# Optimization experiments

Measured on AMD Instinct MI355X. Metric: run time of the kernel, lower is better.

## Reference

```python
import jax, jax.numpy as jnp
import numpy as np

NITER = 3

def fft2c(x):
    x = jnp.fft.ifftshift(x, axes=(-2, -1))
    x = jnp.fft.fft2(x, axes=(-2, -1), norm='ortho')
    return jnp.fft.fftshift(x, axes=(-2, -1))

def ifft2c(x):
    x = jnp.fft.ifftshift(x, axes=(-2, -1))
    x = jnp.fft.ifft2(x, axes=(-2, -1), norm='ortho')
    return jnp.fft.fftshift(x, axes=(-2, -1))

def conv3d(x, w):
    # x: [N, D, H, W, C]; w: [3,3,3,Cin,Cout]; 'same' padding, stride 1, no bias
    return jax.lax.conv_general_dilated(x, w, window_strides=(1, 1, 1), padding='SAME',
                                        dimension_numbers=('NDHWC', 'DHWIO', 'NDHWC'))

def setup_inputs():
    key = jax.random.key(0)
    ks = jax.random.split(key, 16)
    nb, nt, nx, ny = 1, 18, 160, 160
    s = 0.05  # weight scale to keep unrolled iterations numerically tame
    d_real = jax.random.normal(ks[0], (nb, nt, nx, ny), jnp.float32)
    d_imag = jax.random.normal(ks[1], (nb, nt, nx, ny), jnp.float32)
    mask = jax.random.randint(ks[2], (nt, nx, ny), 0, 2, jnp.int32)
    W1 = jax.random.normal(ks[3], (NITER, 3, 3, 3, 2, 16), jnp.float32) * s
    W2 = jax.random.normal(ks[4], (NITER, 3, 3, 3, 16, 16), jnp.float32) * s
    W3 = jax.random.normal(ks[5], (NITER, 3, 3, 3, 16, 16), jnp.float32) * s
    W4 = jax.random.normal(ks[6], (NITER, 3, 3, 3, 16, 16), jnp.float32) * s
    W5 = jax.random.normal(ks[7], (NITER, 3, 3, 3, 16, 16), jnp.float32) * s
    W6 = jax.random.normal(ks[8], (NITER, 3, 3, 3, 16, 2), jnp.float32) * s
    lam1 = jnp.full((NITER,), 0.1, jnp.float32)       # lambda_step init
    lam2 = jnp.full((NITER,), 0.1, jnp.float32)       # lambda_step_2 init
    soft_thr = jnp.full((NITER,), 0.1, jnp.float32)
    thres_coef = jnp.full((NITER,), -2.0, jnp.float32)
    eta = jnp.full((NITER,), 0.01, jnp.float32)
    return dict(d_real=d_real, d_imag=d_imag, mask=mask, W1=W1, W2=W2, W3=W3, W4=W4,
                W5=W5, W6=W6, lam1=lam1, lam2=lam2, soft_thr=soft_thr,
                thres_coef=thres_coef, eta=eta)

def _slr_net(d_real, d_imag, mask, W1, W2, W3, W4, W5, W6, lam1, lam2, soft_thr, thres_coef, eta):
    d = jax.lax.complex(d_real, d_imag)          # [nb,nt,nx,ny] complex64
    m = mask.astype(jnp.complex64)               # [nt,nx,ny], broadcasts over batch
    x_rec = ifft2c(d * m)                        # E^H d
    t = jnp.zeros_like(x_rec)
    beta = jnp.zeros_like(x_rec)
    X_SYM = []
    for i in range(NITER):
        lam = jnp.maximum(lam1[i], 0.0).astype(jnp.complex64)
        lam2c = jnp.maximum(lam2[i], 0.0).astype(jnp.complex64)
        # data-consistency gradient: E^H (E x - d)
        ATAX = ifft2c(m * (m * fft2c(x_rec) - d))
        r_n = x_rec - lam * ATAX + lam2c * (x_rec + beta - t)
        r = jnp.stack([r_n.real, r_n.imag], axis=-1)  # [nb,nt,nx,ny,2]
        x1 = jax.nn.relu(conv3d(r, W1[i]))
        x2 = jax.nn.relu(conv3d(x1, W2[i]))
        x3 = conv3d(x2, W3[i])
        x_soft = jnp.sign(x3) * jax.nn.relu(jnp.abs(x3) - soft_thr[i])
        x4 = jax.nn.relu(conv3d(x_soft, W4[i]))
        x5 = jax.nn.relu(conv3d(x4, W5[i]))
        x6 = conv3d(x5, W6[i])
        x_out = x6 + r
        xs = jax.nn.relu(conv3d(x3, W4[i]))
        xs = jax.nn.relu(conv3d(xs, W5[i]))
        xs = conv3d(xs, W6[i])
        x_sym = xs - r
        x_rec = jax.lax.complex(x_out[..., 0], x_out[..., 1])
        # low-rank step: batched thin SVD with learned singular-value thresholding
        nb_, nt_, nx_, ny_ = x_rec.shape
        M = x_rec.reshape(nb_, nt_, nx_ * ny_)
        U, S, Vh = jnp.linalg.svd(M, full_matrices=False)   # U:[b,nt,nt] S:[b,nt] Vh:[b,nt,nx*ny]
        thres = jax.nn.sigmoid(thres_coef[i]) * S[:, :1]
        S = jax.nn.relu(S - thres)
        t = (U * S[:, None, :].astype(U.dtype)) @ Vh
        t = t.reshape(nb_, nt_, nx_, ny_)
        beta = beta + jnp.maximum(eta[i], 0.0).astype(jnp.complex64) * (x_rec - t)
        X_SYM.append(x_sym)
    return x_rec, jnp.stack(X_SYM)

def reference(d_real, d_imag, mask, W1, W2, W3, W4, W5, W6, lam1, lam2, soft_thr, thres_coef, eta):
    return _slr_net(d_real, d_imag, mask, W1, W2, W3, W4, W5, W6, lam1, lam2, soft_thr, thres_coef, eta)
```

## Files before the change

kernel.cpp:

```cpp
#include <hip/hip_runtime.h>
#include <hip/hip_fp16.h>

#define NT 18
#define NX 160
#define NY 160
#define NPIX (NX*NY)
#define NVOX (NT*NPIX)

typedef _Float16 __attribute__((ext_vector_type(2))) half2t;
typedef _Float16 __attribute__((ext_vector_type(8))) half8t;
typedef float    __attribute__((ext_vector_type(4))) f32x4;
typedef unsigned int u32;
typedef __attribute__((address_space(1))) const u32 gu32;
typedef __attribute__((address_space(3))) u32 lu32;

__global__ void probe_kernel(float* __restrict__ out, int n, float val) {
  int i = blockIdx.x * 256 + threadIdx.x;
  if (i < n) out[i] = val;
}

__global__ void make_g_kernel(float2* __restrict__ G) {
  int idx = blockIdx.x * 256 + threadIdx.x;
  if (idx >= NPIX) return;
  int r = idx / NY, c = idx - (idx / NY) * NY;
  int rs = (r + 80) % 160;
  int cs = (c + 80) % 160;
  int prod = (rs * cs) % 160;
  double ang = -2.0 * 3.14159265358979323846 * (double)prod / 160.0;
  double sc = 0.07905694150420949;
  G[idx] = make_float2((float)(cos(ang) * sc), (float)(sin(ang) * sc));
}

__global__ void zero_kernel(float* __restrict__ p, int n) {
  int i = blockIdx.x * 256 + threadIdx.x;
  if (i < n) p[i] = 0.f;
}

template <int MASKD>
__global__ void fft_pass_last4(const float2* __restrict__ in, float2* __restrict__ out,
                               const float2* __restrict__ G, int conjf,
                               const float* __restrict__ dr, const float* __restrict__ di,
                               const int* __restrict__ maskp) {
  __shared__ float2 rows[4][NY];
  int r0 = blockIdx.x * 4;
  int v = threadIdx.x;
#pragma unroll
  for (int r = 0; r < 4; ++r) {
    size_t idx = (size_t)(r0 + r) * NY + v;
    if (MASKD) {
      float m = (float)maskp[idx];
      rows[r][v] = make_float2(m * dr[idx], m * di[idx]);
    } else {
      rows[r][v] = in[idx];
    }
  }
  __syncthreads();
  float sgn = conjf ? -1.f : 1.f;
  float ar[4] = {0.f, 0.f, 0.f, 0.f}, ai[4] = {0.f, 0.f, 0.f, 0.f};
  for (int k = 0; k < NY; ++k) {
    float2 g = G[k * NY + v];
    float gi = sgn * g.y;
#pragma unroll
    for (int r = 0; r < 4; ++r) {
      float2 a = rows[r][k];
      ar[r] += a.x * g.x - a.y * gi;
      ai[r] += a.x * gi + a.y * g.x;
    }
  }
#pragma unroll
  for (int r = 0; r < 4; ++r)
    out[(size_t)(r0 + r) * NY + v] = make_float2(ar[r], ai[r]);
}

template <int EPI>
__global__ void fft_pass_mid4(const float2* __restrict__ in, void* __restrict__ outv,
                              const float2* __restrict__ G, int conjf,
                              const float* __restrict__ dr, const float* __restrict__ di,
                              const int* __restrict__ maskp,
                              const float2* __restrict__ xrec2, const float2* __restrict__ beta2,
                              const float2* __restrict__ tbuf2,
                              const float* __restrict__ l1p, const float* __restrict__ l2p) {
  __shared__ float2 grow[4][NX];
  int b = (int)blockIdx.x;
  int sb = (b & 7) * 90 + (b >> 3);
  int t = sb / 40;
  int u0 = (sb - t * 40) * 4;
  int v = threadIdx.x;
#pragma unroll
  for (int r = 0; r < 4; ++r) grow[r][v] = G[(u0 + r) * NX + v];
  __syncthreads();
  float sgn = conjf ? -1.f : 1.f;
  float ar[4] = {0.f, 0.f, 0.f, 0.f}, ai[4] = {0.f, 0.f, 0.f, 0.f};
  const float2* base = in + (size_t)t * NPIX;
  for (int j = 0; j < NX; ++j) {
    float2 a = base[j * NY + v];
#pragma unroll
    for (int r = 0; r < 4; ++r) {
      float2 g = grow[r][j];
      float gi = sgn * g.y;
      ar[r] += a.x * g.x - a.y * gi;
      ai[r] += a.x * gi + a.y * g.x;
    }
  }
  float l1 = 0.f, l2 = 0.f;
  if (EPI == 2) { l1 = fmaxf(l1p[0], 0.f); l2 = fmaxf(l2p[0], 0.f); }
#pragma unroll
  for (int r = 0; r < 4; ++r) {
    size_t idx = (size_t)t * NPIX + (size_t)(u0 + r) * NY + v;
    if (EPI == 0) {
      ((float2*)outv)[idx] = make_float2(ar[r], ai[r]);
    } else if (EPI == 1) {
      float m = (float)maskp[idx];
      ((float2*)outv)[idx] = make_float2(m * (m * ar[r] - dr[idx]),
                                         m * (m * ai[r] - di[idx]));
    } else {
      float2 x = xrec2[idx], bb = beta2[idx], tt = tbuf2[idx];
      ((float*)outv)[2 * idx]     = (1.f + l2) * x.x - l1 * ar[r] + l2 * (bb.x - tt.x);
      ((float*)outv)[2 * idx + 1] = (1.f + l2) * x.y - l1 * ai[r] + l2 * (bb.y - tt.y);
    }
  }
}

template <int MODE>
__device__ void eigen_part(const float2* __restrict__ Ain, float* __restrict__ scr,
                           const float* __restrict__ tcp, float2* __restrict__ Wout) {
  __shared__ float Ar[NT][NT], Ai_[NT][NT], Vr[NT][NT], Vi_[NT][NT];
  __shared__ float cS[9], sS[9], erS[9], eiS[9];
  __shared__ int pS[9], qS[9];
  __shared__ float ratio[NT];
  int tid = threadIdx.x;
  for (int idx = tid; idx < NT * NT; idx += 256) {
    int i = idx / NT, j = idx - (idx / NT) * NT;
    if (MODE == 1) {
      float2 a = Ain[idx];
      Ar[i][j] = a.x;
      Ai_[i][j] = (i == j) ? 0.f : a.y;
      Vr[i][j] = (i == j) ? 1.f : 0.f;
      Vi_[i][j] = 0.f;
    } else {
      Ar[i][j] = scr[idx];
      Ai_[i][j] = scr[324 + idx];
      Vr[i][j] = scr[648 + idx];
      Vi_[i][j] = scr[972 + idx];
    }
  }
  __syncthreads();
  for (int sweep = 0; sweep < 2; ++sweep) {
    for (int r = 0; r < NT - 1; ++r) {
      if (tid < 9) {
        int k = tid;
        int a = (r + k) % (NT - 1);
        int b = (k == 0) ? (NT - 1) : (r - k + (NT - 1)) % (NT - 1);
        int p = min(a, b), q = max(a, b);
        pS[k] = p; qS[k] = q;
        float apr = Ar[p][q], api = Ai_[p][q];
        float r2 = apr * apr + api * api;
        float c = 1.f, s = 0.f, er = 1.f, ei = 0.f;
        if (r2 > 1e-28f) {
          float rr = sqrtf(r2);
          float inv_r = 1.f / rr;
          er = apr * inv_r; ei = api * inv_r;
          float th = (Ar[q][q] - Ar[p][p]) * 0.5f * inv_r;
          float tt = (th >= 0.f ? 1.f : -1.f) / (fabsf(th) + sqrtf(th * th + 1.f));
          c = 1.f / sqrtf(tt * tt + 1.f);
          s = tt * c;
        }
        cS[k] = c; sS[k] = s; erS[k] = er; eiS[k] = ei;
      }
      __syncthreads();
      if (tid < 9 * NT) {
        int idx = tid;
        int k = idx / 9, j = idx - (idx / 9) * 9;
        int p = pS[j], q = qS[j];
        float c = cS[j], s = sS[j], er = erS[j], ei = eiS[j];
        float apr = Ar[k][p], api = Ai_[k][p];
        float aqr = Ar[k][q], aqi = Ai_[k][q];
        float eqr = er * aqr + ei * aqi;
        float eqi = er * aqi - ei * aqr;
        Ar[k][p] = c * apr - s * eqr;  Ai_[k][p] = c * api - s * eqi;
        Ar[k][q] = s * apr + c * eqr;  Ai_[k][q] = s * api + c * eqi;
        float vpr = Vr[k][p], vpi = Vi_[k][p];
        float vqr = Vr[k][q], vqi = Vi_[k][q];
        float evr = er * vqr + ei * vqi;
        float evi = er * vqi - ei * vqr;
        Vr[k][p] = c * vpr - s * evr;  Vi_[k][p] = c * vpi - s * evi;
        Vr[k][q] = s * vpr + c * evr;  Vi_[k][q] = s * vpi + c * evi;
      }
      __syncthreads();
      if (tid < 9 * NT) {
        int idx = tid;
        int k = idx / 9, j = idx - (idx / 9) * 9;
        int p = pS[j], q = qS[j];
        float c = cS[j], s = sS[j], er = erS[j], ei = eiS[j];
        float bpr = Ar[p][k], bpi = Ai_[p][k];
        float bqr = Ar[q][k], bqi = Ai_[q][k];
        float ebr = er * bqr - ei * bqi;
        float ebi = er * bqi + ei * bqr;
        Ar[p][k] = c * bpr - s * ebr;  Ai_[p][k] = c * bpi - s * ebi;
        Ar[q][k] = s * bpr + c * ebr;  Ai_[q][k] = s * bpi + c * ebi;
      }
      __syncthreads();
    }
  }
  if (MODE == 3) {
    if (tid == 0) {
      float smax = 0.f;
      for (int k = 0; k < NT; ++k) {
        float sv = sqrtf(fmaxf(Ar[k][k], 0.f));
        ratio[k] = sv;
        smax = fmaxf(smax, sv);
      }
      float sig = 1.f / (1.f + expf(-tcp[0]));
      float thres = sig * smax;
      for (int k = 0; k < NT; ++k) {
        float sv = ratio[k];
        ratio[k] = (sv > thres) ? (sv - thres) / sv : 0.f;
      }
    }
    __syncthreads();
    for (int idx = tid; idx < NT * NT; idx += 256) {
      int i = idx / NT, j = idx - (idx / NT) * NT;
      float wr = 0.f, wi = 0.f;
      for (int k = 0; k < NT; ++k) {
        float rk = ratio[k];
        wr += rk * (Vr[i][k] * Vr[j][k] + Vi_[i][k] * Vi_[j][k]);
        wi += rk * (Vi_[i][k] * Vr[j][k] - Vr[i][k] * Vi_[j][k]);
      }
      Wout[idx] = make_float2(wr, wi);
    }
  } else {
    for (int idx = tid; idx < NT * NT; idx += 256) {
      int i = idx / NT, j = idx - (idx / NT) * NT;
      scr[idx]       = Ar[i][j];
      scr[324 + idx] = Ai_[i][j];
      scr[648 + idx] = Vr[i][j];
      scr[972 + idx] = Vi_[i][j];
    }
  }
}

#define ROWCH 164
#define NROWS 18
#define NCHUNK (NROWS*ROWCH)

template <int COUT, bool RELU, int OUTMODE, bool SOFT, int EIG>
__global__ void __launch_bounds__(256)
conv3d_mfma_kernel(const __half* __restrict__ in_, const float* __restrict__ wts,
                   void* __restrict__ out_, const float* __restrict__ res, float resSign,
                   const float* __restrict__ thrp,
                   const float2* __restrict__ eigA, float* __restrict__ eigScr,
                   const float* __restrict__ tcp, float2* __restrict__ eigW,
                   float* __restrict__ outReal) {
  if constexpr (EIG > 0) {
    if (blockIdx.x == 0) { eigen_part<EIG>(eigA, eigScr, tcp, eigW); return; }
  }
  __shared__ alignas(16) __half lds[NCHUNK * 8];
  const int tid = threadIdx.x;
  const int bid0 = (EIG > 0) ? ((int)blockIdx.x - 1) : (int)blockIdx.x;
  const int bid = (bid0 & 7) * 180 + (bid0 >> 3);
  const int z   = bid / 80;
  const int rem = bid - z * 80;
  const int y0  = (rem >> 1) * 4;
  const int xbase = (rem & 1) * 80;

  const int lane = tid & 63;
  const int wv = tid >> 6;
  const int n = lane & 15;
  const int g = lane >> 4;
  const int sel = g >> 1;
  const int ci = (g & 1) * 8;

  half8t bw[14];
#pragma unroll
  for (int c = 0; c < 14; ++c) {
#pragma unroll
    for (int j = 0; j < 8; ++j) {
      int kg = c * 32 + g * 8 + j;
      float w = (kg < 432 && n < COUT) ? wts[kg * COUT + n] : 0.f;
      bw[c][j] = (_Float16)w;
    }
  }

  if constexpr (!SOFT) {
    half8t zero8 = {0, 0, 0, 0, 0, 0, 0, 0};
    if (tid < 2 * NROWS) {
      int row = tid >> 1, which = tid & 1;
      int off = (xbase == 0) ? which : (162 + which);
      *reinterpret_cast<half8t*>(&lds[(row * ROWCH + off) * 8]) = zero8;
    }
#pragma unroll 1
    for (int row = 0; row < NROWS; ++row) {
      int zz = z - 1 + row / 6;
      int yy = y0 - 1 + row % 6;
      if ((unsigned)zz >= (unsigned)NT || (unsigned)yy >= (unsigned)NX) {
        for (int i = tid; i < ROWCH; i += 256)
          *reinterpret_cast<half8t*>(&lds[(row * ROWCH + i) * 8]) = zero8;
      }
    }
    const int wb = tid & ~63;
#pragma unroll 1
    for (int base = 0; base < NCHUNK; base += 256) {
      int i = base + tid;
      if (i < NCHUNK) {
        int row = i / ROWCH;
        int off = i - row * ROWCH;
        int zz = z - 1 + row / 6;
        int yy = y0 - 1 + row % 6;
        int x = xbase - 1 + (off >> 1);
        bool valid = ((unsigned)zz < (unsigned)NT) && ((unsigned)yy < (unsigned)NX) &&
                     ((unsigned)x < (unsigned)NY);
        if (valid) {
          const __half* src = in_ + ((size_t)((zz * NX + yy) * NY + x)) * 16 + (off & 1) * 8;
          __builtin_amdgcn_global_load_lds(
              (gu32*)(const void*)src,
              (lu32*)(void*)&lds[(size_t)(base + wb) * 8],
              16, 0, 0);
        }
      }
    }
  } else {
    float thr = thrp[0];
    for (int i = tid; i < NCHUNK; i += 256) {
      int row = i / ROWCH;
      int off = i - row * ROWCH;
      int zz = z - 1 + row / 6;
      int yy = y0 - 1 + row % 6;
      int x = xbase - 1 + (off >> 1);
      half8t v = {0, 0, 0, 0, 0, 0, 0, 0};
      if ((unsigned)zz < (unsigned)NT && (unsigned)yy < (unsigned)NX &&
          (unsigned)x < (unsigned)NY) {
        v = *reinterpret_cast<const half8t*>(
              in_ + ((size_t)((zz * NX + yy) * NY + x)) * 16 + (off & 1) * 8);
#pragma unroll
        for (int e = 0; e < 8; ++e) {
          float f = (float)v[e];
          v[e] = (_Float16)copysignf(fmaxf(fabsf(f) - thr, 0.f), f);
        }
      }
      *reinterpret_cast<half8t*>(&lds[(size_t)i * 8]) = v;
    }
  }
  __syncthreads();

  const int yloc = wv;
#pragma unroll 1
  for (int t = 0; t < 5; ++t) {
    int xloc = t * 16;

    f32x4 acc = {0.f, 0.f, 0.f, 0.f};
#pragma unroll
    for (int c = 0; c < 14; ++c) {
      const int t0 = 2 * c, t1 = 2 * c + 1;
      const int dz0 = t0 / 9, dy0 = (t0 / 3) % 3, dx0 = t0 % 3;
      const int dz1 = t1 / 9, dy1 = (t1 / 3) % 3, dx1 = t1 % 3;
      half8t a = {0, 0, 0, 0, 0, 0, 0, 0};
      if (c < 13 || !sel) {
        int dz = sel ? dz1 : dz0;
        int dy = sel ? dy1 : dy0;
        int dx = sel ? dx1 : dx0;
        int rowi = dz * 6 + yloc + dy;
        int slot = xloc + n + dx;
        int aoff = rowi * (ROWCH * 8) + slot * 16 + ci;
        a = *reinterpret_cast<const half8t*>(&lds[aoff]);
      }
      acc = __builtin_amdgcn_mfma_f32_16x16x32_f16(a, bw[c], acc, 0, 0, 0);
    }

    size_t vb = ((size_t)(z * NX) + (y0 + yloc)) * NY + xbase + xloc;
    if (n < COUT) {
#pragma unroll
      for (int r = 0; r < 4; ++r) {
        float v = acc[r];
        size_t oidx = (vb + g * 4 + r) * COUT + n;
        if (res) v += resSign * res[oidx];
        if (RELU) v = fmaxf(v, 0.f);
        if (OUTMODE == 1) ((__half*)out_)[oidx] = __float2half(v);
        else {
          ((float*)out_)[oidx] = v;
          if (COUT == 2 && outReal && n == 0) outReal[vb + g * 4 + r] = v;
        }
      }
    }
  }
}

template <bool RELU>
__global__ void __launch_bounds__(256)
conv3d_mfma2in_kernel(const float* __restrict__ in_, const float* __restrict__ wts,
                      __half* __restrict__ out_) {
  __shared__ alignas(8) __half lds2[12 * 324];
  const int tid = threadIdx.x;
  const int bid0 = (int)blockIdx.x;
  const int bid = (bid0 & 7) * 180 + (bid0 >> 3);
  const int z  = bid / 80;
  const int y0 = (bid - z * 80) * 2;
  const int lane = tid & 63;
  const int wv = tid >> 6;
  const int n = lane & 15;
  const int g = lane >> 4;

  half8t bw[2];
#pragma unroll
  for (int c = 0; c < 2; ++c) {
#pragma unroll
    for (int j = 0; j < 8; ++j) {
      int k = c * 32 + g * 8 + j;
      float w = (k < 54) ? wts[k * 16 + n] : 0.f;
      bw[c][j] = (_Float16)w;
    }
  }

  for (int i = tid; i < 12 * 162; i += 256) {
    int row = i / 162;
    int vox = i - row * 162;
    int zz = z - 1 + (row >> 2);
    int yy = y0 - 1 + (row & 3);
    int xx = vox - 1;
    half2t v2 = {(_Float16)0.f, (_Float16)0.f};
    if ((unsigned)zz < (unsigned)NT && (unsigned)yy < (unsigned)NX && (unsigned)xx < (unsigned)NY) {
      float2 f = reinterpret_cast<const float2*>(in_)[(size_t)(zz * NX + yy) * NY + xx];
      v2[0] = (_Float16)f.x;
      v2[1] = (_Float16)f.y;
    }
    *reinterpret_cast<half2t*>(&lds2[i * 2]) = v2;
  }
  __syncthreads();

#pragma unroll 1
  for (int t = 0; t < 5; ++t) {
    int tl = wv * 5 + t;
    int yloc = (tl >= 10) ? 1 : 0;
    int x0 = (tl - yloc * 10) * 16;
    f32x4 acc = {0.f, 0.f, 0.f, 0.f};
#pragma unroll
    for (int c = 0; c < 2; ++c) {
      half8t a = {0, 0, 0, 0, 0, 0, 0, 0};
#pragma unroll
      for (int u = 0; u < 4; ++u) {
        int tap = c * 16 + g * 4 + u;
        if (tap < 27) {
          int dz = tap / 9, dy = (tap / 3) % 3, dx = tap % 3;
          int rowi = dz * 4 + yloc + dy;
          half2t p = *reinterpret_cast<const half2t*>(&lds2[rowi * 324 + (x0 + n + dx) * 2]);
          a[2 * u] = p[0];
          a[2 * u + 1] = p[1];
        }
      }
      acc = __builtin_amdgcn_mfma_f32_16x16x32_f16(a, bw[c], acc, 0, 0, 0);
    }
    size_t vb = ((size_t)(z * NX) + (y0 + yloc)) * NY + x0;
#pragma unroll
    for (int r = 0; r < 4; ++r) {
      float v = acc[r];
      if (RELU) v = fmaxf(v, 0.f);
      out_[(vb + g * 4 + r) * 16 + n] = __float2half(v);
    }
  }
}

__global__ void gram_kernel(const float2* __restrict__ M, float2* __restrict__ A) {
  int b = blockIdx.x;
  int i = 0;
  while (b >= NT - i) { b -= NT - i; ++i; }
  int j = i + b;
  int tid = threadIdx.x;
  float sr = 0.f, si = 0.f;
  for (int p = tid; p < NPIX; p += 256) {
    float2 a = M[(size_t)i * NPIX + p];
    float2 c = M[(size_t)j * NPIX + p];
    sr += a.x * c.x + a.y * c.y;
    si += a.y * c.x - a.x * c.y;
  }
  __shared__ float rs[256], is_[256];
  rs[tid] = sr; is_[tid] = si;
  __syncthreads();
  for (int s = 128; s > 0; s >>= 1) {
    if (tid < s) { rs[tid] += rs[tid + s]; is_[tid] += is_[tid + s]; }
    __syncthreads();
  }
  if (tid == 0) {
    A[i * NT + j] = make_float2(rs[0], is_[0]);
    if (i != j) A[j * NT + i] = make_float2(rs[0], -is_[0]);
  }
}

__global__ void svd_apply_kernel(const float2* __restrict__ M, const float2* __restrict__ Wm,
                                 float2* __restrict__ t, float2* __restrict__ beta,
                                 const float* __restrict__ etap) {
  __shared__ float2 W[NT * NT];
  int tid = threadIdx.x;
  for (int i = tid; i < NT * NT; i += 256) W[i] = Wm[i];
  __syncthreads();
  int p = blockIdx.x * 256 + tid;
  float eta = fmaxf(etap[0], 0.f);
  float2 m[NT];
#pragma unroll
  for (int j = 0; j < NT; ++j) m[j] = M[(size_t)j * NPIX + p];
#pragma unroll
  for (int i = 0; i < NT; ++i) {
    float tr = 0.f, ti = 0.f;
#pragma unroll
    for (int j = 0; j < NT; ++j) {
      float2 w = W[i * NT + j];
      tr += w.x * m[j].x - w.y * m[j].y;
      ti += w.x * m[j].y + w.y * m[j].x;
    }
    t[(size_t)i * NPIX + p] = make_float2(tr, ti);
    float2 b = beta[(size_t)i * NPIX + p];
    b.x += eta * (m[i].x - tr);
    b.y += eta * (m[i].y - ti);
    beta[(size_t)i * NPIX + p] = b;
  }
}

extern "C" void kernel_launch(void* const* d_in, const int* in_sizes, int n_in,
                              void* d_out, int out_size, void* d_ws, size_t ws_size,
                              hipStream_t stream) {
  const float* d_real    = (const float*)d_in[0];
  const float* d_imag    = (const float*)d_in[1];
  const int*   mask      = (const int*)d_in[2];
  const float* W1        = (const float*)d_in[3];
  const float* W2        = (const float*)d_in[4];
  const float* W3        = (const float*)d_in[5];
  const float* W4        = (const float*)d_in[6];
  const float* W5        = (const float*)d_in[7];
  const float* W6        = (const float*)d_in[8];
  const float* lam1      = (const float*)d_in[9];
  const float* lam2      = (const float*)d_in[10];
  const float* soft_thr  = (const float*)d_in[11];
  const float* thres_c   = (const float*)d_in[12];
  const float* eta       = (const float*)d_in[13];
  float* out = (float*)d_out;
  (void)in_sizes; (void)n_in;

  const size_t NEEDED = 59400000ull;
  if (ws_size < NEEDED) {
    probe_kernel<<<(out_size + 255) / 256, 256, 0, stream>>>(out, out_size,
                                                             (float)(ws_size >> 20));
    return;
  }

  char* wp_ = (char*)d_ws;
  auto alloc = [&](size_t bytes) {
    char* r = wp_;
    wp_ += (bytes + 255) & ~(size_t)255;
    return r;
  };
  float2* G      = (float2*)alloc((size_t)NPIX * sizeof(float2));
  float2* xrec   = (float2*)alloc((size_t)NVOX * sizeof(float2));
  float2* tbuf   = (float2*)alloc((size_t)NVOX * sizeof(float2));
  float2* beta   = (float2*)alloc((size_t)NVOX * sizeof(float2));
  float*  Rf     = (float*)alloc((size_t)NVOX * 2 * sizeof(float));
  __half* Af     = (__half*)alloc((size_t)NVOX * 16 * sizeof(__half));
  __half* Bf     = (__half*)alloc((size_t)NVOX * 16 * sizeof(__half));
  __half* Cf     = (__half*)alloc((size_t)NVOX * 16 * sizeof(__half));
  float2* Agram  = (float2*)alloc((size_t)NT * NT * sizeof(float2));
  float2* Wmat   = (float2*)alloc((size_t)NT * NT * sizeof(float2));
  float*  EigScr = (float*)alloc(1296 * sizeof(float));
  float2* T1 = (float2*)Af;
  float2* T2 = (float2*)Bf;

  make_g_kernel<<<100, 256, 0, stream>>>(G);
  zero_kernel<<<7200, 256, 0, stream>>>((float*)tbuf, 4 * NVOX);

  fft_pass_last4<1><<<720, 160, 0, stream>>>(nullptr, T2, G, 1, d_real, d_imag, mask);
  fft_pass_mid4<0><<<720, 160, 0, stream>>>(T2, xrec, G, 1, nullptr, nullptr, nullptr,
                                            nullptr, nullptr, nullptr, nullptr, nullptr);

  for (int i = 0; i < 3; ++i) {
    fft_pass_last4<0><<<720, 160, 0, stream>>>(xrec, T1, G, 0, nullptr, nullptr, nullptr);
    fft_pass_mid4<1><<<720, 160, 0, stream>>>(T1, T2, G, 0, d_real, d_imag, mask,
                                              nullptr, nullptr, nullptr, nullptr, nullptr);
    fft_pass_last4<0><<<720, 160, 0, stream>>>(T2, T1, G, 1, nullptr, nullptr, nullptr);
    fft_pass_mid4<2><<<720, 160, 0, stream>>>(T1, Rf, G, 1, nullptr, nullptr, nullptr,
                                              xrec, beta, tbuf, lam1 + i, lam2 + i);
    conv3d_mfma2in_kernel<true><<<1440, 256, 0, stream>>>(Rf, W1 + (size_t)i * 864, Af);
    conv3d_mfma_kernel<16, true, 1, false, 0><<<1440, 256, 0, stream>>>(
        Af, W2 + (size_t)i * 6912, Bf, nullptr, 0.f, nullptr,
        nullptr, nullptr, nullptr, nullptr, nullptr);
    conv3d_mfma_kernel<16, false, 1, false, 0><<<1440, 256, 0, stream>>>(
        Bf, W3 + (size_t)i * 6912, Cf, nullptr, 0.f, nullptr,
        nullptr, nullptr, nullptr, nullptr, nullptr);
    conv3d_mfma_kernel<16, true, 1, true, 0><<<1440, 256, 0, stream>>>(
        Cf, W4 + (size_t)i * 6912, Bf, nullptr, 0.f, soft_thr + i,
        nullptr, nullptr, nullptr, nullptr, nullptr);
    conv3d_mfma_kernel<16, true, 1, false, 0><<<1440, 256, 0, stream>>>(
        Bf, W5 + (size_t)i * 6912, Af, nullptr, 0.f, nullptr,
        nullptr, nullptr, nullptr, nullptr, nullptr);

    if (i < 2) {
      conv3d_mfma_kernel<2, false, 0, false, 0><<<1440, 256, 0, stream>>>(
          Af, W6 + (size_t)i * 864, (float*)xrec, Rf, 1.f, nullptr,
          nullptr, nullptr, nullptr, nullptr, nullptr);
      gram_kernel<<<171, 256, 0, stream>>>((const float2*)xrec, Agram);
      conv3d_mfma_kernel<16, true, 1, false, 1><<<1441, 256, 0, stream>>>(
          Cf, W4 + (size_t)i * 6912, Bf, nullptr, 0.f, nullptr,
          Agram, EigScr, thres_c + i, Wmat, nullptr);
      conv3d_mfma_kernel<16, true, 1, false, 2><<<1441, 256, 0, stream>>>(
          Bf, W5 + (size_t)i * 6912, Af, nullptr, 0.f, nullptr,
          Agram, EigScr, thres_c + i, Wmat, nullptr);
      conv3d_mfma_kernel<2, false, 0, false, 3><<<1441, 256, 0, stream>>>(
          Af, W6 + (size_t)i * 864, out + 460800 + (size_t)921600 * i, Rf, -1.f, nullptr,
          Agram, EigScr, thres_c + i, Wmat, nullptr);
      svd_apply_kernel<<<100, 256, 0, stream>>>((const float2*)xrec, Wmat, tbuf, beta, eta + i);
    } else {
      conv3d_mfma_kernel<2, false, 0, false, 0><<<1440, 256, 0, stream>>>(
          Af, W6 + (size_t)i * 864, (float*)xrec, Rf, 1.f, nullptr,
          nullptr, nullptr, nullptr, nullptr, out);
      conv3d_mfma_kernel<16, true, 1, false, 0><<<1440, 256, 0, stream>>>(
          Cf, W4 + (size_t)i * 6912, Bf, nullptr, 0.f, nullptr,
          nullptr, nullptr, nullptr, nullptr, nullptr);
      conv3d_mfma_kernel<16, true, 1, false, 0><<<1440, 256, 0, stream>>>(
          Bf, W5 + (size_t)i * 6912, Af, nullptr, 0.f, nullptr,
          nullptr, nullptr, nullptr, nullptr, nullptr);
      conv3d_mfma_kernel<2, false, 0, false, 0><<<1440, 256, 0, stream>>>(
          Af, W6 + (size_t)i * 864, out + 460800 + (size_t)921600 * i, Rf, -1.f, nullptr,
          nullptr, nullptr, nullptr, nullptr, nullptr);
    }
  }
}
```

Baseline: 1.219 ms.

## Pair the two conv branches of the last iteration into shared 2880-block launches

In the final iteration, the soft-threshold branch and the symmetric branch run the same W4/W5/W6 convolutions on different inputs. Each pair is now merged into one launch with doubled grid, where the upper half of the blocks switches input, output and residual sign. An extra fp16 buffer is allocated so the two chains do not overwrite each other. This cuts three launches and fills the GPU better, at the cost of a runtime branch on the soft-threshold path and a larger workspace requirement.

```diff
diff --git a/kernel.cpp b/kernel.cpp
--- a/kernel.cpp
+++ b/kernel.cpp
@@ -242,21 +242,31 @@
 #define ROWCH 164
 #define NROWS 18
 #define NCHUNK (NROWS*ROWCH)
-
-template <int COUT, bool RELU, int OUTMODE, bool SOFT, int EIG>
+#define NBLK 1440
+
+template <int COUT, bool RELU, int OUTMODE, bool SOFT, int EIG, bool PAIRED>
 __global__ void __launch_bounds__(256)
 conv3d_mfma_kernel(const __half* __restrict__ in_, const float* __restrict__ wts,
                    void* __restrict__ out_, const float* __restrict__ res, float resSign,
                    const float* __restrict__ thrp,
                    const float2* __restrict__ eigA, float* __restrict__ eigScr,
                    const float* __restrict__ tcp, float2* __restrict__ eigW,
-                   float* __restrict__ outReal) {
+                   float* __restrict__ outReal,
+                   const __half* __restrict__ in1, void* __restrict__ out1, float resSign1) {
   if constexpr (EIG > 0) {
     if (blockIdx.x == 0) { eigen_part<EIG>(eigA, eigScr, tcp, eigW); return; }
   }
   __shared__ alignas(16) __half lds[NCHUNK * 8];
   const int tid = threadIdx.x;
-  const int bid0 = (EIG > 0) ? ((int)blockIdx.x - 1) : (int)blockIdx.x;
+  int bid0 = (EIG > 0) ? ((int)blockIdx.x - 1) : (int)blockIdx.x;
+  const __half* inp = in_;
+  void* outp = out_;
+  float rs = resSign;
+  bool dosoft = SOFT;
+  float* oreal = outReal;
+  if (PAIRED && bid0 >= NBLK) {
+    bid0 -= NBLK; inp = in1; outp = out1; rs = resSign1; dosoft = false; oreal = nullptr;
+  }
   const int bid = (bid0 & 7) * 180 + (bid0 >> 3);
   const int z   = bid / 80;
   const int rem = bid - z * 80;
@@ -281,7 +291,7 @@
     }
   }
 
-  if constexpr (!SOFT) {
+  if (!dosoft) {
     half8t zero8 = {0, 0, 0, 0, 0, 0, 0, 0};
     if (tid < 2 * NROWS) {
       int row = tid >> 1, which = tid & 1;
@@ -310,7 +320,7 @@
         bool valid = ((unsigned)zz < (unsigned)NT) && ((unsigned)yy < (unsigned)NX) &&
                      ((unsigned)x < (unsigned)NY);
         if (valid) {
-          const __half* src = in_ + ((size_t)((zz * NX + yy) * NY + x)) * 16 + (off & 1) * 8;
+          const __half* src = inp + ((size_t)((zz * NX + yy) * NY + x)) * 16 + (off & 1) * 8;
           __builtin_amdgcn_global_load_lds(
               (gu32*)(const void*)src,
               (lu32*)(void*)&lds[(size_t)(base + wb) * 8],
@@ -319,7 +329,7 @@
       }
     }
   } else {
-    float thr = thrp[0];
+    float thr = SOFT ? thrp[0] : 0.f;
     for (int i = tid; i < NCHUNK; i += 256) {
       int row = i / ROWCH;
       int off = i - row * ROWCH;
@@ -330,7 +340,7 @@
       if ((unsigned)zz < (unsigned)NT && (unsigned)yy < (unsigned)NX &&
           (unsigned)x < (unsigned)NY) {
         v = *reinterpret_cast<const half8t*>(
-              in_ + ((size_t)((zz * NX + yy) * NY + x)) * 16 + (off & 1) * 8);
+              inp + ((size_t)((zz * NX + yy) * NY + x)) * 16 + (off & 1) * 8);
 #pragma unroll
         for (int e = 0; e < 8; ++e) {
           float f = (float)v[e];
@@ -372,12 +382,12 @@
       for (int r = 0; r < 4; ++r) {
         float v = acc[r];
         size_t oidx = (vb + g * 4 + r) * COUT + n;
-        if (res) v += resSign * res[oidx];
+        if (res) v += rs * res[oidx];
         if (RELU) v = fmaxf(v, 0.f);
-        if (OUTMODE == 1) ((__half*)out_)[oidx] = __float2half(v);
+        if (OUTMODE == 1) ((__half*)outp)[oidx] = __float2half(v);
         else {
-          ((float*)out_)[oidx] = v;
-          if (COUT == 2 && outReal && n == 0) outReal[vb + g * 4 + r] = v;
+          ((float*)outp)[oidx] = v;
+          if (COUT == 2 && oreal && n == 0) oreal[vb + g * 4 + r] = v;
         }
       }
     }
@@ -533,7 +543,7 @@
   float* out = (float*)d_out;
   (void)in_sizes; (void)n_in;
 
-  const size_t NEEDED = 59400000ull;
+  const size_t NEEDED = 74200000ull;
   if (ws_size < NEEDED) {
     probe_kernel<<<(out_size + 255) / 256, 256, 0, stream>>>(out, out_size,
                                                              (float)(ws_size >> 20));
@@ -554,6 +564,7 @@
   __half* Af     = (__half*)alloc((size_t)NVOX * 16 * sizeof(__half));
   __half* Bf     = (__half*)alloc((size_t)NVOX * 16 * sizeof(__half));
   __half* Cf     = (__half*)alloc((size_t)NVOX * 16 * sizeof(__half));
+  __half* Df     = (__half*)alloc((size_t)NVOX * 16 * sizeof(__half));
   float2* Agram  = (float2*)alloc((size_t)NT * NT * sizeof(float2));
   float2* Wmat   = (float2*)alloc((size_t)NT * NT * sizeof(float2));
   float*  EigScr = (float*)alloc(1296 * sizeof(float));
@@ -575,47 +586,45 @@
     fft_pass_mid4<2><<<720, 160, 0, stream>>>(T1, Rf, G, 1, nullptr, nullptr, nullptr,
                                               xrec, beta, tbuf, lam1 + i, lam2 + i);
     conv3d_mfma2in_kernel<true><<<1440, 256, 0, stream>>>(Rf, W1 + (size_t)i * 864, Af);
-    conv3d_mfma_kernel<16, true, 1, false, 0><<<1440, 256, 0, stream>>>(
+    conv3d_mfma_kernel<16, true, 1, false, 0, false><<<1440, 256, 0, stream>>>(
         Af, W2 + (size_t)i * 6912, Bf, nullptr, 0.f, nullptr,
-        nullptr, nullptr, nullptr, nullptr, nullptr);
-    conv3d_mfma_kernel<16, false, 1, false, 0><<<1440, 256, 0, stream>>>(
+        nullptr, nullptr, nullptr, nullptr, nullptr, nullptr, nullptr, 0.f);
+    conv3d_mfma_kernel<16, false, 1, false, 0, false><<<1440, 256, 0, stream>>>(
         Bf, W3 + (size_t)i * 6912, Cf, nullptr, 0.f, nullptr,
-        nullptr, nullptr, nullptr, nullptr, nullptr);
-    conv3d_mfma_kernel<16, true, 1, true, 0><<<1440, 256, 0, stream>>>(
-        Cf, W4 + (size_t)i * 6912, Bf, nullptr, 0.f, soft_thr + i,
-        nullptr, nullptr, nullptr, nullptr, nullptr);
-    conv3d_mfma_kernel<16, true, 1, false, 0><<<1440, 256, 0, stream>>>(
-        Bf, W5 + (size_t)i * 6912, Af, nullptr, 0.f, nullptr,
-        nullptr, nullptr, nullptr, nullptr, nullptr);
+        nullptr, nullptr, nullptr, nullptr, nullptr, nullptr, nullptr, 0.f);
 
     if (i < 2) {
-      conv3d_mfma_kernel<2, false, 0, false, 0><<<1440, 256, 0, stream>>>(
+      conv3d_mfma_kernel<16, true, 1, true, 0, false><<<1440, 256, 0, stream>>>(
+          Cf, W4 + (size_t)i * 6912, Bf, nullptr, 0.f, soft_thr + i,
+          nullptr, nullptr, nullptr, nullptr, nullptr, nullptr, nullptr, 0.f);
+      conv3d_mfma_kernel<16, true, 1, false, 0, false><<<1440, 256, 0, stream>>>(
+          Bf, W5 + (size_t)i * 6912, Af, nullptr, 0.f, nullptr,
+          nullptr, nullptr, nullptr, nullptr, nullptr, nullptr, nullptr, 0.f);
+      conv3d_mfma_kernel<2, false, 0, false, 0, false><<<1440, 256, 0, stream>>>(
           Af, W6 + (size_t)i * 864, (float*)xrec, Rf, 1.f, nullptr,
-          nullptr, nullptr, nullptr, nullptr, nullptr);
+          nullptr, nullptr, nullptr, nullptr, nullptr, nullptr, nullptr, 0.f);
       gram_kernel<<<171, 256, 0, stream>>>((const float2*)xrec, Agram);
-      conv3d_mfma_kernel<16, true, 1, false, 1><<<1441, 256, 0, stream>>>(
+      conv3d_mfma_kernel<16, true, 1, false, 1, false><<<1441, 256, 0, stream>>>(
           Cf, W4 + (size_t)i * 6912, Bf, nullptr, 0.f, nullptr,
-          Agram, EigScr, thres_c + i, Wmat, nullptr);
-      conv3d_mfma_kernel<16, true, 1, false, 2><<<1441, 256, 0, stream>>>(
+          Agram, EigScr, thres_c + i, Wmat, nullptr, nullptr, nullptr, 0.f);
+      conv3d_mfma_kernel<16, true, 1, false, 2, false><<<1441, 256, 0, stream>>>(
           Bf, W5 + (size_t)i * 6912, Af, nullptr, 0.f, nullptr,
-          Agram, EigScr, thres_c + i, Wmat, nullptr);
-      conv3d_mfma_kernel<2, false, 0, false, 3><<<1441, 256, 0, stream>>>(
+          Agram, EigScr, thres_c + i, Wmat, nullptr, nullptr, nullptr, 0.f);
+      conv3d_mfma_kernel<2, false, 0, false, 3, false><<<1441, 256, 0, stream>>>(
           Af, W6 + (size_t)i * 864, out + 460800 + (size_t)921600 * i, Rf, -1.f, nullptr,
-          Agram, EigScr, thres_c + i, Wmat, nullptr);
+          Agram, EigScr, thres_c + i, Wmat, nullptr, nullptr, nullptr, 0.f);
       svd_apply_kernel<<<100, 256, 0, stream>>>((const float2*)xrec, Wmat, tbuf, beta, eta + i);
     } else {
-      conv3d_mfma_kernel<2, false, 0, false, 0><<<1440, 256, 0, stream>>>(
+      conv3d_mfma_kernel<16, true, 1, true, 0, true><<<2880, 256, 0, stream>>>(
+          Cf, W4 + (size_t)i * 6912, Bf, nullptr, 0.f, soft_thr + i,
+          nullptr, nullptr, nullptr, nullptr, nullptr, Cf, Df, 0.f);
+      conv3d_mfma_kernel<16, true, 1, false, 0, true><<<2880, 256, 0, stream>>>(
+          Bf, W5 + (size_t)i * 6912, Af, nullptr, 0.f, nullptr,
+          nullptr, nullptr, nullptr, nullptr, nullptr, Df, Cf, 0.f);
+      conv3d_mfma_kernel<2, false, 0, false, 0, true><<<2880, 256, 0, stream>>>(
           Af, W6 + (size_t)i * 864, (float*)xrec, Rf, 1.f, nullptr,
-          nullptr, nullptr, nullptr, nullptr, out);
-      conv3d_mfma_kernel<16, true, 1, false, 0><<<1440, 256, 0, stream>>>(
-          Cf, W4 + (size_t)i * 6912, Bf, nullptr, 0.f, nullptr,
-          nullptr, nullptr, nullptr, nullptr, nullptr);
-      conv3d_mfma_kernel<16, true, 1, false, 0><<<1440, 256, 0, stream>>>(
-          Bf, W5 + (size_t)i * 6912, Af, nullptr, 0.f, nullptr,
-          nullptr, nullptr, nullptr, nullptr, nullptr);
-      conv3d_mfma_kernel<2, false, 0, false, 0><<<1440, 256, 0, stream>>>(
-          Af, W6 + (size_t)i * 864, out + 460800 + (size_t)921600 * i, Rf, -1.f, nullptr,
-          nullptr, nullptr, nullptr, nullptr, nullptr);
-    }
-  }
-}
+          nullptr, nullptr, nullptr, nullptr, out,
+          Cf, out + 460800 + (size_t)921600 * i, -1.f);
+    }
+  }
+}
```

Result: no change. 1.199 ms (-1.6%).
